# Kernel optimization log

Hardware: AMD Instinct MI355X
Metric: run time of the kernel (lower is better)

Reference implementation:

```python
import jax, jax.numpy as jnp
import numpy as np

DEPTH = 4
DIM = 128
M_DIM = 16
FEAT_DIM = 10
K = 12
CLAMP = 2.0
B, N = 4, 2048
EI = 2 * DIM + 1  # edge_input_dim = feats_i + feats_j + rel_dist


def setup_inputs() -> dict:
    key = jax.random.key(0)
    ks = jax.random.split(key, 16)
    def p(k, shape, s=0.05):
        return jax.random.normal(k, shape, dtype=jnp.float32) * s
    inp = dict(
        feats=jax.random.normal(ks[0], (B, N, FEAT_DIM), dtype=jnp.float32),
        coords=jax.random.normal(ks[1], (B, N, 3), dtype=jnp.float32) * 3.0,
        mask=jnp.ones((B, N), dtype=bool),
        emb_w=p(ks[2], (FEAT_DIM, DIM)), emb_b=p(ks[3], (DIM,)),
        ew1=p(ks[4], (DEPTH, EI, 2 * EI)), eb1=p(ks[5], (DEPTH, 2 * EI)),
        ew2=p(ks[6], (DEPTH, 2 * EI, M_DIM)), eb2=p(ks[7], (DEPTH, M_DIM)),
        cw1=p(ks[8], (DEPTH, M_DIM, 4 * M_DIM)), cb1=p(ks[9], (DEPTH, 4 * M_DIM)),
        cw2=p(ks[10], (DEPTH, 4 * M_DIM, 1)), cb2=p(ks[11], (DEPTH, 1)),
        cscale=jnp.full((DEPTH, 1), 1e-2, dtype=jnp.float32),  # CoorsNorm scale_init
        nw1=p(ks[12], (DEPTH, DIM + M_DIM, 2 * DIM)), nb1=p(ks[13], (DEPTH, 2 * DIM)),
        nw2=p(ks[14], (DEPTH, 2 * DIM, DIM)), nb2=p(ks[15], (DEPTH, DIM)),
    )
    return inp


def _egnn_layer(feats, coors, mask, lp):
    ew1, eb1, ew2, eb2, cw1, cb1, cw2, cb2, cscale, nw1, nb1, nw2, nb2 = lp
    # pairwise relative coords / squared distances
    rel = coors[:, :, None, :] - coors[:, None, :, :]            # (B,N,N,3)
    dist = jnp.sum(rel * rel, axis=-1)                           # (B,N,N)
    pm = mask[:, :, None] & mask[:, None, :]
    ranking = jnp.where(pm, dist, 1e5)
    _, nbhd = jax.lax.top_k(-ranking, K)                         # (B,N,K) smallest dists
    rel_k = jnp.take_along_axis(rel, nbhd[..., None], axis=2)    # (B,N,K,3)
    dist_k = jnp.take_along_axis(dist, nbhd, axis=2)             # (B,N,K)
    feats_j = jax.vmap(lambda f, i: f[i])(feats, nbhd)           # (B,N,K,D)
    mask_j = jnp.take_along_axis(jnp.broadcast_to(mask[:, None, :], dist.shape), nbhd, axis=2)
    m2 = mask[:, :, None] & mask_j                               # (B,N,K)
    feats_i = jnp.broadcast_to(feats[:, :, None, :], feats_j.shape)
    edge_in = jnp.concatenate([feats_i, feats_j, dist_k[..., None]], axis=-1)  # (B,N,K,EI)
    m_ij = jax.nn.silu(jax.nn.silu(edge_in @ ew1 + eb1) @ ew2 + eb2)           # (B,N,K,M)
    # coordinate update (E(n)-equivariant)
    w = (jax.nn.silu(m_ij @ cw1 + cb1) @ cw2 + cb2)[..., 0]      # (B,N,K)
    nrm = jnp.sqrt(jnp.sum(rel_k * rel_k, axis=-1, keepdims=True))
    rel_n = rel_k / jnp.maximum(nrm, 1e-8) * cscale              # CoorsNorm
    w = jnp.clip(jnp.where(m2, w, 0.0), -CLAMP, CLAMP)
    coors_out = coors + jnp.einsum('bik,bikc->bic', w, rel_n)
    # node update (residual)
    m_i = jnp.sum(jnp.where(m2[..., None], m_ij, 0.0), axis=2)   # (B,N,M)
    node_in = jnp.concatenate([feats, m_i], axis=-1)
    feats_out = jax.nn.silu(node_in @ nw1 + nb1) @ nw2 + nb2 + feats
    return feats_out, coors_out


def reference(feats, coords, mask, emb_w, emb_b, ew1, eb1, ew2, eb2, cw1, cb1, cw2, cb2, cscale, nw1, nb1, nw2, nb2):
    h = feats @ emb_w + emb_b                                    # continuous feature embedding
    c = coords
    for l in range(DEPTH):
        lp = (ew1[l], eb1[l], ew2[l], eb2[l], cw1[l], cb1[l], cw2[l], cb2[l],
              cscale[l], nw1[l], nb1[l], nw2[l], nb2[l])
        h, c = _egnn_layer(h, c, mask, lp)
    mf = mask.astype(h.dtype)
    out = jnp.sum(h * mf[..., None], axis=1) / jnp.sum(mf, axis=1, keepdims=True)  # (B,DIM)
    return out
```

## Files before the change

kernel.cpp:

```cpp
#include <hip/hip_runtime.h>
#include <hip/hip_bf16.h>
#include <math.h>

#define NB 4
#define NN 2048
#define DIMF 128
#define MD 16
#define KK 12
#define NODES (NB*NN)

typedef __attribute__((ext_vector_type(8))) short bf16x8;
typedef __attribute__((ext_vector_type(4))) float f32x4;

__device__ __forceinline__ float silu_f(float x) {
    return x * __builtin_amdgcn_rcpf(1.0f + __expf(-x));
}

__device__ __forceinline__ short f2bf(float x) {
    unsigned u = __float_as_uint(x);
    unsigned r = (u + 0x7FFFu + ((u >> 16) & 1u)) >> 16;
    return (short)r;
}

__device__ __forceinline__ short2 pkbf(float a, float b) {
    union { __hip_bfloat162 h; short2 s; } u;
    u.h = __float22bfloat162_rn(make_float2(a, b));
    return u.s;
}

__device__ __forceinline__ void upk8(uint4 u, float* f) {
    f[0] = __uint_as_float(u.x << 16); f[1] = __uint_as_float(u.x & 0xFFFF0000u);
    f[2] = __uint_as_float(u.y << 16); f[3] = __uint_as_float(u.y & 0xFFFF0000u);
    f[4] = __uint_as_float(u.z << 16); f[5] = __uint_as_float(u.z & 0xFFFF0000u);
    f[6] = __uint_as_float(u.w << 16); f[7] = __uint_as_float(u.w & 0xFFFF0000u);
}

__device__ __forceinline__ void knn_body(const float* __restrict__ coords,
                                         int* __restrict__ nbhd,
                                         int b2, int tid, float* sc) {
    int batch = b2 >> 9;
    int qbase = (b2 & 511) << 2;
    const float* cb = coords + (size_t)batch * NN * 3;
    const float4* cb4 = (const float4*)cb;
    int wv = tid >> 6, lane = tid & 63;
    int ql = qbase + wv;
    float qx = cb[3 * ql], qy = cb[3 * ql + 1], qz = cb[3 * ql + 2];
    float kd[KK]; int ki[KK];
#pragma unroll
    for (int r = 0; r < KK; ++r) { kd[r] = 3.0e38f; ki[r] = -1; }
#pragma unroll
    for (int half = 0; half < 2; ++half) {
#pragma unroll
        for (int t = 0; t < 3; ++t) {
            int e = tid + t * 256;
            ((float4*)sc)[e] = cb4[half * 768 + e];
        }
        __syncthreads();
#pragma unroll 4
        for (int jj = 0; jj < 16; ++jj) {
            int jl = (jj << 6) + lane;
            float dx = sc[3 * jl] - qx, dy = sc[3 * jl + 1] - qy, dz = sc[3 * jl + 2] - qz;
            float d2 = dx * dx + dy * dy + dz * dz;
            float cv = d2; int cix = (half << 10) + jl;
#pragma unroll
            for (int r = 0; r < KK; ++r) {
                bool sw = cv < kd[r];
                float tv = sw ? kd[r] : cv; int ti = sw ? ki[r] : cix;
                kd[r] = sw ? cv : kd[r];    ki[r] = sw ? cix : ki[r];
                cv = tv; cix = ti;
            }
        }
        __syncthreads();
    }
    int* out = nbhd + ((size_t)batch * NN + ql) * KK;
#pragma unroll
    for (int pass = 0; pass < KK; ++pass) {
        float mv = kd[0]; int mj = ki[0];
#pragma unroll
        for (int o = 1; o < 64; o <<= 1) {
            float ov = __shfl_xor(mv, o);
            int   oj = __shfl_xor(mj, o);
            if (ov < mv || (ov == mv && oj < mj)) { mv = ov; mj = oj; }
        }
        if (lane == 0) out[pass] = batch * NN + mj;
        if (kd[0] == mv && ki[0] == mj) {
#pragma unroll
            for (int r = 0; r < KK - 1; ++r) { kd[r] = kd[r + 1]; ki[r] = ki[r + 1]; }
            kd[KK - 1] = 3.0e38f;
        }
    }
}

template<typename AT, typename OT, int ACT, int RPW>
__device__ __forceinline__ void mgemm_body(
    const AT* __restrict__ A, int lda,
    const float* __restrict__ Bm, int ldb,
    OT* __restrict__ C, int ldc,
    const float* __restrict__ bias,
    const float* __restrict__ resid, int ldr,
    int N, int K, int bx, int by, int tid,
    unsigned short (*sA)[40], unsigned short (*sBt)[40])
{
    constexpr bool AF32 = (sizeof(AT) == 4);
    int lane = tid & 63, w = tid >> 6, quad = lane >> 4, l16 = lane & 15;
    int rowBase = by * (RPW * 64);
    int colBase = bx * 64;
    f32x4 acc[RPW][4];
#pragma unroll
    for (int rt = 0; rt < RPW; ++rt)
#pragma unroll
        for (int ct = 0; ct < 4; ++ct) acc[rt][ct] = (f32x4){0.f, 0.f, 0.f, 0.f};

    int kend = (K + 31) >> 5;
    for (int kc = 0; kc < kend; ++kc) {
        int k0 = kc * 32;
        if constexpr (AF32) {
#pragma unroll
            for (int p = 0; p < RPW * 2; ++p) {
                int e = tid + p * 256;
                int r = e >> 3, kq = e & 7, kg = k0 + kq * 4;
                short4 sv = {0, 0, 0, 0};
                if (kg + 4 <= K) {
                    float4 v = *(const float4*)&A[(size_t)(rowBase + r) * lda + kg];
                    short2 a = pkbf(v.x, v.y), b = pkbf(v.z, v.w);
                    sv = make_short4(a.x, a.y, b.x, b.y);
                }
                *(short4*)&sA[r][kq * 4] = sv;
            }
        } else {
#pragma unroll
            for (int p = 0; p < RPW; ++p) {
                int e = tid + p * 256;
                int r = e >> 2, k8 = (e & 3) * 8, kg = k0 + k8;
                uint4 v = {0u, 0u, 0u, 0u};
                if (kg + 8 <= K)
                    v = *(const uint4*)&A[(size_t)(rowBase + r) * lda + kg];
                *(uint4*)&sA[r][k8] = v;
            }
        }
#pragma unroll
        for (int p = 0; p < 4; ++p) {
            int e = tid + p * 256;
            int kk = e >> 5, c2 = (e & 31) * 2, kg = k0 + kk;
            int c0 = colBase + c2;
            float v0 = (kg < K && c0 < N)     ? Bm[(size_t)kg * ldb + c0]     : 0.0f;
            float v1 = (kg < K && c0 + 1 < N) ? Bm[(size_t)kg * ldb + c0 + 1] : 0.0f;
            sBt[c2][kk]     = (unsigned short)f2bf(v0);
            sBt[c2 + 1][kk] = (unsigned short)f2bf(v1);
        }
        __syncthreads();
        bf16x8 a[RPW], b[4];
#pragma unroll
        for (int rt = 0; rt < RPW; ++rt)
            a[rt] = *(const bf16x8*)&sA[w * (RPW * 16) + rt * 16 + l16][quad * 8];
#pragma unroll
        for (int ct = 0; ct < 4; ++ct)
            b[ct] = *(const bf16x8*)&sBt[ct * 16 + l16][quad * 8];
#pragma unroll
        for (int rt = 0; rt < RPW; ++rt)
#pragma unroll
            for (int ct = 0; ct < 4; ++ct)
                acc[rt][ct] = __builtin_amdgcn_mfma_f32_16x16x32_bf16(a[rt], b[ct], acc[rt][ct], 0, 0, 0);
        __syncthreads();
    }
#pragma unroll
    for (int rt = 0; rt < RPW; ++rt) {
#pragma unroll
        for (int ct = 0; ct < 4; ++ct) {
            int col = colBase + ct * 16 + l16;
            if (col < N) {
                float bv = bias ? bias[col] : 0.0f;
#pragma unroll
                for (int r = 0; r < 4; ++r) {
                    int row = rowBase + w * (RPW * 16) + rt * 16 + quad * 4 + r;
                    float v = acc[rt][ct][r] + bv;
                    if (ACT) v = silu_f(v);
                    if (resid) v += resid[(size_t)row * ldr + col];
                    if constexpr (sizeof(OT) == 4)
                        C[(size_t)row * ldc + col] = v;
                    else
                        C[(size_t)row * ldc + col] = (OT)f2bf(v);
                }
            }
        }
    }
}

template<typename AT, typename OT, int ACT, int RPW>
__global__ __launch_bounds__(256) void mgemm_kernel(
    const AT* __restrict__ A, int lda,
    const float* __restrict__ Bm, int ldb,
    OT* __restrict__ C, int ldc,
    const float* __restrict__ bias,
    const float* __restrict__ resid, int ldr,
    int N, int K)
{
    __shared__ __attribute__((aligned(16))) unsigned short sA[RPW * 64][40];
    __shared__ __attribute__((aligned(16))) unsigned short sBt[64][40];
    mgemm_body<AT, OT, ACT, RPW>(A, lda, Bm, ldb, C, ldc, bias, resid, ldr,
                                 N, K, blockIdx.x, blockIdx.y, threadIdx.x, sA, sBt);
}

__global__ __launch_bounds__(256) void embed_knn_kernel(
    const float* __restrict__ feats, const float* __restrict__ w,
    const float* __restrict__ b, float* __restrict__ h,
    const float* __restrict__ coords, int* __restrict__ nbhd)
{
    __shared__ __attribute__((aligned(16))) float sc[3072];
    int tid = threadIdx.x;
    if ((int)blockIdx.x < 2048) {
        knn_body(coords, nbhd, blockIdx.x, tid, sc);
    } else {
        int idx = ((int)blockIdx.x - 2048) * 256 + tid;
        int n = idx >> 7, d = idx & 127;
        const float* fr = feats + n * 10;
        float acc = b[d];
#pragma unroll
        for (int f = 0; f < 10; ++f) acc = fmaf(fr[f], w[f * 128 + d], acc);
        h[idx] = acc;
    }
}

__global__ __launch_bounds__(256) void mlp1knn_kernel(
    const float* __restrict__ nodein_, const float* __restrict__ nw1l,
    unsigned short* __restrict__ t1b, const float* __restrict__ nb1l,
    const float* __restrict__ coordsN, int* __restrict__ nbhd, int knnb)
{
    __shared__ __attribute__((aligned(16))) char smem[15360];
    int tid = threadIdx.x;
    if ((int)blockIdx.x < knnb) {
        knn_body(coordsN, nbhd, blockIdx.x, tid, (float*)smem);
    } else {
        int q = (int)blockIdx.x - knnb;
        mgemm_body<float, unsigned short, 1, 1>(
            nodein_, 144, nw1l, 256, t1b, 256, nb1l, nullptr, 0,
            256, 144, q & 3, q >> 2, tid,
            (unsigned short(*)[40])smem, (unsigned short(*)[40])(smem + 5120));
    }
}

__global__ __launch_bounds__(256) void pq_gemm_kernel(
    const float* __restrict__ A,
    const float* __restrict__ B1, const float* __restrict__ B2,
    unsigned short* __restrict__ PQb,
    const float* __restrict__ bias)
{
    __shared__ __attribute__((aligned(16))) unsigned short sA[128][40];
    __shared__ __attribute__((aligned(16))) unsigned short sBt[64][40];
    int tid = threadIdx.x;
    int lane = tid & 63, w = tid >> 6, quad = lane >> 4, l16 = lane & 15;
    int rowBase = blockIdx.y * 128;
    int colBase = blockIdx.x * 64;
    f32x4 acc[2][4];
#pragma unroll
    for (int rt = 0; rt < 2; ++rt)
#pragma unroll
        for (int ct = 0; ct < 4; ++ct) acc[rt][ct] = (f32x4){0.f, 0.f, 0.f, 0.f};

#pragma unroll
    for (int kc = 0; kc < 4; ++kc) {
        int k0 = kc * 32;
#pragma unroll
        for (int p = 0; p < 4; ++p) {
            int e = tid + p * 256;
            int r = e >> 3, kq = e & 7;
            float4 v = *(const float4*)&A[(size_t)(rowBase + r) * 128 + k0 + kq * 4];
            short2 a = pkbf(v.x, v.y), b = pkbf(v.z, v.w);
            *(short4*)&sA[r][kq * 4] = make_short4(a.x, a.y, b.x, b.y);
        }
#pragma unroll
        for (int p = 0; p < 4; ++p) {
            int e = tid + p * 256;
            int kk = e >> 5, c2 = (e & 31) * 2, kg = k0 + kk;
            int c0 = colBase + c2;
            float v0 = 0.0f, v1 = 0.0f;
            if (c0 < 1028) {
                const float* Bp = (c0 < 514) ? B1 : B2;
                int cc = (c0 < 514) ? c0 : c0 - 514;
                v0 = Bp[(size_t)kg * 514 + cc];
            }
            if (c0 + 1 < 1028) {
                const float* Bp = (c0 + 1 < 514) ? B1 : B2;
                int cc = (c0 + 1 < 514) ? c0 + 1 : c0 + 1 - 514;
                v1 = Bp[(size_t)kg * 514 + cc];
            }
            sBt[c2][kk]     = (unsigned short)f2bf(v0);
            sBt[c2 + 1][kk] = (unsigned short)f2bf(v1);
        }
        __syncthreads();
        bf16x8 a[2], b[4];
#pragma unroll
        for (int rt = 0; rt < 2; ++rt)
            a[rt] = *(const bf16x8*)&sA[w * 32 + rt * 16 + l16][quad * 8];
#pragma unroll
        for (int ct = 0; ct < 4; ++ct)
            b[ct] = *(const bf16x8*)&sBt[ct * 16 + l16][quad * 8];
#pragma unroll
        for (int rt = 0; rt < 2; ++rt)
#pragma unroll
            for (int ct = 0; ct < 4; ++ct)
                acc[rt][ct] = __builtin_amdgcn_mfma_f32_16x16x32_bf16(a[rt], b[ct], acc[rt][ct], 0, 0, 0);
        __syncthreads();
    }
#pragma unroll
    for (int rt = 0; rt < 2; ++rt) {
#pragma unroll
        for (int ct = 0; ct < 4; ++ct) {
            int col = colBase + ct * 16 + l16;
            if (col < 1028) {
                bool isP = col < 514;
                int oc = isP ? col : col + 14;
                float bv = isP ? bias[col] : 0.0f;
#pragma unroll
                for (int r = 0; r < 4; ++r) {
                    int row = rowBase + w * 32 + rt * 16 + quad * 4 + r;
                    PQb[(size_t)row * 1056 + oc] = (unsigned short)f2bf(acc[rt][ct][r] + bv);
                }
            }
        }
    }
}

__global__ __launch_bounds__(256, 8) void edge_kernel(
    const unsigned short* __restrict__ PQ, const int* __restrict__ nbhd,
    const float* __restrict__ cin, float* __restrict__ cout,
    float* __restrict__ nodein, const float* __restrict__ hin,
    const float* __restrict__ wrow,
    const float* __restrict__ ew2l,
    const float* __restrict__ cw1l,
    const float* __restrict__ eb2l,
    const float* __restrict__ cb1l,
    const float* __restrict__ cw2l,
    const float* __restrict__ cb2l,
    const float* __restrict__ cscalel)
{
    __shared__ __attribute__((aligned(16))) unsigned short sB[17][64][8];
    __shared__ __attribute__((aligned(16))) float swl[544];
    int tid = threadIdx.x;

    for (int idx = tid; idx < 8704; idx += 256) {
        int kc = idx >> 9, ln = (idx >> 3) & 63, j = idx & 7;
        int k = kc * 32 + ((ln >> 4) << 3) + j, n = ln & 15;
        sB[kc][ln][j] = (k < 514) ? (unsigned short)f2bf(ew2l[k * 16 + n]) : (unsigned short)0;
    }
    for (int idx = tid; idx < 544; idx += 256)
        swl[idx] = (idx < 514) ? wrow[idx] : 0.0f;
    __syncthreads();

    int lane = tid & 63, wv = tid >> 6;
    int quad = lane >> 4, e = lane & 15;
    int bid = blockIdx.x;
    int rr8 = bid & 7, bsw = rr8 >> 1;
    int wsw = ((bid >> 3) << 1) | (rr8 & 1);
    int nodeBase = bsw * 2048 + wsw * 4;
    int i = nodeBase + wv;
    int ec = e < KK ? e : KK - 1;
    int j = nbhd[i * KK + ec];
    float cix = cin[i * 3], ciy = cin[i * 3 + 1], ciz = cin[i * 3 + 2];
    float rx = cix - cin[j * 3], ry = ciy - cin[j * 3 + 1], rz = ciz - cin[j * 3 + 2];
    float d2 = rx * rx + ry * ry + rz * rz;

    const unsigned short* Pp = PQ + (size_t)i * 1056 + quad * 8;
    const unsigned short* Qp = PQ + (size_t)j * 1056 + 528 + quad * 8;

    uint4 pb[3], qb[3];
    pb[0] = *(const uint4*)Pp;
    qb[0] = *(const uint4*)Qp;
    pb[1] = *(const uint4*)(Pp + 32);
    qb[1] = *(const uint4*)(Qp + 32);

    f32x4 acc = {0.0f, 0.0f, 0.0f, 0.0f};
#pragma unroll
    for (int kc = 0; kc < 16; ++kc) {
        int cur = kc % 3, nx = (kc + 2) % 3;
        if (kc < 14) {
            pb[nx] = *(const uint4*)(Pp + (kc + 2) * 32);
            qb[nx] = *(const uint4*)(Qp + (kc + 2) * 32);
        }
        float p[8], q[8];
        upk8(pb[cur], p); upk8(qb[cur], q);
        float4 w0 = *(const float4*)&swl[quad * 8 + kc * 32];
        float4 w1 = *(const float4*)&swl[quad * 8 + kc * 32 + 4];
        float h0 = silu_f(fmaf(d2, w0.x, p[0] + q[0]));
        float h1 = silu_f(fmaf(d2, w0.y, p[1] + q[1]));
        float h2 = silu_f(fmaf(d2, w0.z, p[2] + q[2]));
        float h3 = silu_f(fmaf(d2, w0.w, p[3] + q[3]));
        float h4 = silu_f(fmaf(d2, w1.x, p[4] + q[4]));
        float h5 = silu_f(fmaf(d2, w1.y, p[5] + q[5]));
        float h6 = silu_f(fmaf(d2, w1.z, p[6] + q[6]));
        float h7 = silu_f(fmaf(d2, w1.w, p[7] + q[7]));
        bf16x8 af;
        short2 r0 = pkbf(h0, h1), r1 = pkbf(h2, h3), r2 = pkbf(h4, h5), r3 = pkbf(h6, h7);
        af[0] = r0.x; af[1] = r0.y; af[2] = r1.x; af[3] = r1.y;
        af[4] = r2.x; af[5] = r2.y; af[6] = r3.x; af[7] = r3.y;
        bf16x8 bf = *(const bf16x8*)&sB[kc][lane][0];
        acc = __builtin_amdgcn_mfma_f32_16x16x32_bf16(af, bf, acc, 0, 0, 0);
    }
    {
        unsigned up = *(const unsigned*)(PQ + (size_t)i * 1056 + 512);
        unsigned uq = *(const unsigned*)(PQ + (size_t)j * 1056 + 528 + 512);
        bf16x8 af = {0, 0, 0, 0, 0, 0, 0, 0};
        if (quad == 0) {
            float px = __uint_as_float(up << 16), py = __uint_as_float(up & 0xFFFF0000u);
            float qx = __uint_as_float(uq << 16), qy = __uint_as_float(uq & 0xFFFF0000u);
            af[0] = f2bf(silu_f(fmaf(d2, swl[512], px + qx)));
            af[1] = f2bf(silu_f(fmaf(d2, swl[513], py + qy)));
        }
        bf16x8 bf = *(const bf16x8*)&sB[16][lane][0];
        acc = __builtin_amdgcn_mfma_f32_16x16x32_bf16(af, bf, acc, 0, 0, 0);
    }

    float eb = eb2l[lane & 15];
    float m[4];
#pragma unroll
    for (int r = 0; r < 4; ++r) {
        float v = silu_f(acc[r] + eb);
        m[r] = (quad == 3) ? 0.0f : v;
    }
    float ms = m[0] + m[1] + m[2] + m[3];
    ms += __shfl_xor(ms, 16);
    ms += __shfl_xor(ms, 32);
    if (quad == 0) nodein[(size_t)i * 144 + 128 + (lane & 15)] = ms;

    __syncthreads();
    unsigned short* sCp = (unsigned short*)sB;
    unsigned short* mp  = (unsigned short*)((char*)sB + 4096);
    float* wp           = (float*)((char*)sB + 6144);
    for (int idx = tid; idx < 2048; idx += 256) {
        int nb = idx >> 9, ln = (idx >> 3) & 63, jj = idx & 7;
        int c = ((ln >> 4) << 3) + jj, n = nb * 16 + (ln & 15);
        sCp[idx] = (c < 16) ? (unsigned short)f2bf(cw1l[c * 64 + n]) : (unsigned short)0;
    }
#pragma unroll
    for (int r = 0; r < 4; ++r)
        mp[wv * 256 + (quad * 4 + r) * 16 + (lane & 15)] = (unsigned short)f2bf(m[r]);
    __syncthreads();

    bf16x8 af2 = {0, 0, 0, 0, 0, 0, 0, 0};
    if (quad < 2) af2 = *(const bf16x8*)(mp + wv * 256 + (lane & 15) * 16 + quad * 8);
    float wpart[4] = {0.0f, 0.0f, 0.0f, 0.0f};
#pragma unroll
    for (int nb = 0; nb < 4; ++nb) {
        bf16x8 cf = *(const bf16x8*)(sCp + ((nb * 64 + lane) << 3));
        f32x4 z = {0.0f, 0.0f, 0.0f, 0.0f};
        f32x4 t = __builtin_amdgcn_mfma_f32_16x16x32_bf16(af2, cf, z, 0, 0, 0);
        int d = nb * 16 + (lane & 15);
        float cb = cb1l[d], cw = cw2l[d];
#pragma unroll
        for (int r = 0; r < 4; ++r)
            wpart[r] = fmaf(silu_f(t[r] + cb), cw, wpart[r]);
    }
#pragma unroll
    for (int o = 1; o < 16; o <<= 1)
#pragma unroll
        for (int r = 0; r < 4; ++r) wpart[r] += __shfl_xor(wpart[r], o);
    if ((lane & 15) == 0) {
        float cb2v = cb2l[0];
#pragma unroll
        for (int r = 0; r < 4; ++r) {
            float w = wpart[r] + cb2v;
            w = fminf(fmaxf(w, -2.0f), 2.0f);
            wp[wv * 16 + quad * 4 + r] = w;
        }
    }
    __syncthreads();

    float we = wp[wv * 16 + e];
    float f = (quad == 0 && e < KK)
                  ? we * cscalel[0] / fmaxf(sqrtf(d2), 1e-8f) : 0.0f;
    float cxs = f * rx, cys = f * ry, czs = f * rz;
#pragma unroll
    for (int o = 1; o < 16; o <<= 1) {
        cxs += __shfl_xor(cxs, o);
        cys += __shfl_xor(cys, o);
        czs += __shfl_xor(czs, o);
    }
    if (lane == 0) {
        cout[i * 3]     = cix + cxs;
        cout[i * 3 + 1] = ciy + cys;
        cout[i * 3 + 2] = ciz + czs;
    }

    if (tid < 128) {
        int rr = tid >> 5, c4 = (tid & 31) * 4;
        *(float4*)&nodein[(size_t)(nodeBase + rr) * 144 + c4] =
            *(const float4*)&hin[(size_t)(nodeBase + rr) * 128 + c4];
    }
}

__global__ __launch_bounds__(256) void final1_kernel(const float* __restrict__ h,
                                                     float* __restrict__ part) {
    int b = blockIdx.x >> 5, sl = blockIdx.x & 31;
    int d = threadIdx.x & 127, half = threadIdx.x >> 7;
    const float* hp = h + ((size_t)b * NN + sl * 64) * DIMF;
    float acc = 0.0f;
    for (int n = half; n < 64; n += 2) acc += hp[(size_t)n * DIMF + d];
    __shared__ float red[256];
    red[threadIdx.x] = acc;
    __syncthreads();
    if (half == 0) part[(size_t)blockIdx.x * DIMF + d] = red[d] + red[d + 128];
}

__global__ __launch_bounds__(128) void final2_kernel(const float* __restrict__ part,
                                                     float* __restrict__ out) {
    int b = blockIdx.x, d = threadIdx.x;
    float acc = 0.0f;
#pragma unroll
    for (int s = 0; s < 32; ++s) acc += part[(size_t)(b * 32 + s) * DIMF + d];
    out[b * DIMF + d] = acc * (1.0f / NN);
}

extern "C" void kernel_launch(void* const* d_in, const int* in_sizes, int n_in,
                              void* d_out, int out_size, void* d_ws, size_t ws_size,
                              hipStream_t stream) {
    const float* feats  = (const float*)d_in[0];
    const float* coords = (const float*)d_in[1];
    const float* emb_w  = (const float*)d_in[3];
    const float* emb_b  = (const float*)d_in[4];
    const float* ew1    = (const float*)d_in[5];
    const float* eb1    = (const float*)d_in[6];
    const float* ew2    = (const float*)d_in[7];
    const float* eb2    = (const float*)d_in[8];
    const float* cw1    = (const float*)d_in[9];
    const float* cb1    = (const float*)d_in[10];
    const float* cw2    = (const float*)d_in[11];
    const float* cb2    = (const float*)d_in[12];
    const float* cscale = (const float*)d_in[13];
    const float* nw1    = (const float*)d_in[14];
    const float* nb1    = (const float*)d_in[15];
    const float* nw2    = (const float*)d_in[16];
    const float* nb2    = (const float*)d_in[17];

    char* ws = (char*)d_ws;
    float* h0     = (float*)(ws + 0);
    float* h1     = (float*)(ws + 4194304);
    float* c0     = (float*)(ws + 8388608);
    float* c1     = (float*)(ws + 8486912);
    int*   nbhd   = (int*)  (ws + 8585216);
    float* nodein = (float*)(ws + 8978432);
    unsigned short* PQb = (unsigned short*)(ws + 13697024);
    unsigned short* t1b = (unsigned short*)(ws + 31457280);
    float* part   = (float*)(ws + 13697024);

    float* hbuf[2] = {h0, h1};
    float* cbuf[2] = {c0, c1};

    embed_knn_kernel<<<6144, 256, 0, stream>>>(feats, emb_w, emb_b, h0, coords, nbhd);

    for (int l = 0; l < 4; ++l) {
        const float* hin  = hbuf[l & 1];
        float*       hout = hbuf[(l + 1) & 1];
        const float* cin  = (l == 0) ? coords : cbuf[(l - 1) & 1];
        float*       cout = cbuf[l & 1];
        const float* ew1l = ew1 + (size_t)l * 257 * 514;

        pq_gemm_kernel<<<dim3(17, 64), 256, 0, stream>>>(
            hin, ew1l, ew1l + 128 * 514, PQb, eb1 + l * 514);

        edge_kernel<<<NODES / 4, 256, 0, stream>>>(PQb, nbhd, cin, cout, nodein, hin,
            ew1l + 256 * 514, ew2 + (size_t)l * 514 * 16, cw1 + (size_t)l * 1024,
            eb2 + l * 16, cb1 + l * 64, cw2 + l * 64, cb2 + l, cscale + l);

        int knnb = (l < 3) ? 2048 : 0;
        mlp1knn_kernel<<<knnb + 512, 256, 0, stream>>>(
            nodein, nw1 + (size_t)l * 144 * 256, t1b, nb1 + l * 256,
            cout, nbhd, knnb);

        mgemm_kernel<unsigned short, float, 0, 1><<<dim3(2, 128), 256, 0, stream>>>(
            t1b, 256, nw2 + (size_t)l * 256 * 128, 128, hout, 128,
            nb2 + l * 128, hin, 128, 128, 256);
    }

    final1_kernel<<<NB * 32, 256, 0, stream>>>(hbuf[0], part);
    final2_kernel<<<NB, 128, 0, stream>>>(part, (float*)d_out);
}
```

Before: 601.2 us.

## Pack edges densely across three waves in edge kernel instead of padding per node

The edge kernel previously gave each node its own 64-lane wave, with 16 MFMA rows holding only 12 real edges, so a quarter of the edge work was padding. It now launches 192 threads, and the three waves cover 48 contiguous edges, which is four nodes of twelve edges each, so every MFMA row is a real edge. Because a node's edges can now span waves, the per-node message sums and coordinate updates move to LDS-based reductions done by a subset of threads. The cost is extra LDS traffic and another serial reduction step, plus a different occupancy target in the launch bounds.

```diff
diff --git a/kernel.cpp b/kernel.cpp
--- a/kernel.cpp
+++ b/kernel.cpp
@@ -321,7 +321,7 @@
     }
 }
 
-__global__ __launch_bounds__(256, 8) void edge_kernel(
+__global__ __launch_bounds__(192, 6) void edge_kernel(
     const unsigned short* __restrict__ PQ, const int* __restrict__ nbhd,
     const float* __restrict__ cin, float* __restrict__ cout,
     float* __restrict__ nodein, const float* __restrict__ hin,
@@ -338,24 +338,26 @@
     __shared__ __attribute__((aligned(16))) float swl[544];
     int tid = threadIdx.x;
 
-    for (int idx = tid; idx < 8704; idx += 256) {
+    for (int idx = tid; idx < 8704; idx += 192) {
         int kc = idx >> 9, ln = (idx >> 3) & 63, j = idx & 7;
         int k = kc * 32 + ((ln >> 4) << 3) + j, n = ln & 15;
         sB[kc][ln][j] = (k < 514) ? (unsigned short)f2bf(ew2l[k * 16 + n]) : (unsigned short)0;
     }
-    for (int idx = tid; idx < 544; idx += 256)
+    for (int idx = tid; idx < 544; idx += 192)
         swl[idx] = (idx < 514) ? wrow[idx] : 0.0f;
     __syncthreads();
 
-    int lane = tid & 63, wv = tid >> 6;
-    int quad = lane >> 4, e = lane & 15;
+    int lane = tid & 63, w = tid >> 6;
+    int quad = lane >> 4, e16 = lane & 15;
+    int eloc = w * 16 + e16;
+    int nloc = eloc / 12;
+    int k12 = eloc - nloc * 12;
     int bid = blockIdx.x;
     int rr8 = bid & 7, bsw = rr8 >> 1;
     int wsw = ((bid >> 3) << 1) | (rr8 & 1);
     int nodeBase = bsw * 2048 + wsw * 4;
-    int i = nodeBase + wv;
-    int ec = e < KK ? e : KK - 1;
-    int j = nbhd[i * KK + ec];
+    int i = nodeBase + nloc;
+    int j = nbhd[i * KK + k12];
     float cix = cin[i * 3], ciy = cin[i * 3 + 1], ciz = cin[i * 3 + 2];
     float rx = cix - cin[j * 3], ry = ciy - cin[j * 3 + 1], rz = ciz - cin[j * 3 + 2];
     float d2 = rx * rx + ry * ry + rz * rz;
@@ -410,41 +412,51 @@
         acc = __builtin_amdgcn_mfma_f32_16x16x32_bf16(af, bf, acc, 0, 0, 0);
     }
 
-    float eb = eb2l[lane & 15];
+    float eb = eb2l[e16];
     float m[4];
 #pragma unroll
-    for (int r = 0; r < 4; ++r) {
-        float v = silu_f(acc[r] + eb);
-        m[r] = (quad == 3) ? 0.0f : v;
-    }
-    float ms = m[0] + m[1] + m[2] + m[3];
-    ms += __shfl_xor(ms, 16);
-    ms += __shfl_xor(ms, 32);
-    if (quad == 0) nodein[(size_t)i * 144 + 128 + (lane & 15)] = ms;
+    for (int r = 0; r < 4; ++r) m[r] = silu_f(acc[r] + eb);
 
     __syncthreads();
     unsigned short* sCp = (unsigned short*)sB;
-    unsigned short* mp  = (unsigned short*)((char*)sB + 4096);
-    float* wp           = (float*)((char*)sB + 6144);
-    for (int idx = tid; idx < 2048; idx += 256) {
+    unsigned short* mbf = (unsigned short*)((char*)sB + 4096);
+    float* mf32         = (float*)((char*)sB + 5632);
+    float* reld2        = (float*)((char*)sB + 8704);
+    float* wall         = (float*)((char*)sB + 9472);
+    for (int idx = tid; idx < 2048; idx += 192) {
         int nb = idx >> 9, ln = (idx >> 3) & 63, jj = idx & 7;
         int c = ((ln >> 4) << 3) + jj, n = nb * 16 + (ln & 15);
         sCp[idx] = (c < 16) ? (unsigned short)f2bf(cw1l[c * 64 + n]) : (unsigned short)0;
     }
 #pragma unroll
-    for (int r = 0; r < 4; ++r)
-        mp[wv * 256 + (quad * 4 + r) * 16 + (lane & 15)] = (unsigned short)f2bf(m[r]);
+    for (int r = 0; r < 4; ++r) {
+        int row = w * 16 + quad * 4 + r;
+        mbf[row * 16 + e16] = (unsigned short)f2bf(m[r]);
+        mf32[row * 16 + e16] = m[r];
+    }
+    if (quad == 0) {
+        int eo = (w * 16 + e16) * 4;
+        reld2[eo] = rx; reld2[eo + 1] = ry; reld2[eo + 2] = rz; reld2[eo + 3] = d2;
+    }
     __syncthreads();
 
+    if (tid < 64) {
+        int n = tid >> 4, ch = tid & 15;
+        float s = 0.0f;
+#pragma unroll
+        for (int ke = 0; ke < KK; ++ke) s += mf32[(n * 12 + ke) * 16 + ch];
+        nodein[(size_t)(nodeBase + n) * 144 + 128 + ch] = s;
+    }
+
     bf16x8 af2 = {0, 0, 0, 0, 0, 0, 0, 0};
-    if (quad < 2) af2 = *(const bf16x8*)(mp + wv * 256 + (lane & 15) * 16 + quad * 8);
+    if (quad < 2) af2 = *(const bf16x8*)&mbf[(w * 16 + e16) * 16 + quad * 8];
     float wpart[4] = {0.0f, 0.0f, 0.0f, 0.0f};
 #pragma unroll
     for (int nb = 0; nb < 4; ++nb) {
         bf16x8 cf = *(const bf16x8*)(sCp + ((nb * 64 + lane) << 3));
         f32x4 z = {0.0f, 0.0f, 0.0f, 0.0f};
         f32x4 t = __builtin_amdgcn_mfma_f32_16x16x32_bf16(af2, cf, z, 0, 0, 0);
-        int d = nb * 16 + (lane & 15);
+        int d = nb * 16 + e16;
         float cb = cb1l[d], cw = cw2l[d];
 #pragma unroll
         for (int r = 0; r < 4; ++r)
@@ -454,31 +466,30 @@
     for (int o = 1; o < 16; o <<= 1)
 #pragma unroll
         for (int r = 0; r < 4; ++r) wpart[r] += __shfl_xor(wpart[r], o);
-    if ((lane & 15) == 0) {
+    if (e16 == 0) {
         float cb2v = cb2l[0];
 #pragma unroll
         for (int r = 0; r < 4; ++r) {
-            float w = wpart[r] + cb2v;
-            w = fminf(fmaxf(w, -2.0f), 2.0f);
-            wp[wv * 16 + quad * 4 + r] = w;
+            float ww = wpart[r] + cb2v;
+            ww = fminf(fmaxf(ww, -2.0f), 2.0f);
+            wall[w * 16 + quad * 4 + r] = ww;
         }
     }
     __syncthreads();
 
-    float we = wp[wv * 16 + e];
-    float f = (quad == 0 && e < KK)
-                  ? we * cscalel[0] / fmaxf(sqrtf(d2), 1e-8f) : 0.0f;
-    float cxs = f * rx, cys = f * ry, czs = f * rz;
-#pragma unroll
-    for (int o = 1; o < 16; o <<= 1) {
-        cxs += __shfl_xor(cxs, o);
-        cys += __shfl_xor(cys, o);
-        czs += __shfl_xor(czs, o);
-    }
-    if (lane == 0) {
-        cout[i * 3]     = cix + cxs;
-        cout[i * 3 + 1] = ciy + cys;
-        cout[i * 3 + 2] = ciz + czs;
+    if (tid < 12) {
+        int n = tid / 3, c = tid - n * 3;
+        float cs = cscalel[0];
+        float s = 0.0f;
+#pragma unroll
+        for (int ke = 0; ke < KK; ++ke) {
+            int eo = (n * 12 + ke) * 4;
+            float d2e = reld2[eo + 3];
+            float f = wall[n * 12 + ke] * cs * __builtin_amdgcn_rcpf(fmaxf(sqrtf(d2e), 1e-8f));
+            s = fmaf(f, reld2[eo + c], s);
+        }
+        int node = nodeBase + n;
+        cout[node * 3 + c] = cin[node * 3 + c] + s;
     }
 
     if (tid < 128) {
@@ -557,7 +568,7 @@
         pq_gemm_kernel<<<dim3(17, 64), 256, 0, stream>>>(
             hin, ew1l, ew1l + 128 * 514, PQb, eb1 + l * 514);
 
-        edge_kernel<<<NODES / 4, 256, 0, stream>>>(PQb, nbhd, cin, cout, nodein, hin,
+        edge_kernel<<<NODES / 4, 192, 0, stream>>>(PQb, nbhd, cin, cout, nodein, hin,
             ew1l + 256 * 514, ew2 + (size_t)l * 514 * 16, cw1 + (size_t)l * 1024,
             eb2 + l * 16, cb1 + l * 64, cw2 + l * 64, cb2 + l, cscale + l);
 
```

Measured after the change: 595.3 us. No clear change (-1.0%).
